# Kernel tuning notes

Measured on AMD Instinct MI355X. Metric: run time of the kernel, lower is better.

Reference implementation:

```python
import jax, jax.numpy as jnp
import numpy as np

N = 4096
IN_DIM = 256
HID = 64
HEADS = 4
OUT_DIM = 64
NEG = -9e15


def setup_inputs() -> dict:
    key = jax.random.key(0)
    ks = jax.random.split(key, 12)
    h = jax.random.normal(ks[0], (N, IN_DIM), dtype=jnp.float32)
    adj = jax.random.randint(ks[1], (N, N), 0, 2, dtype=jnp.int32)
    # per-head GATLayer params (W: Linear(input_dim, hid) with bias; a: Linear(2*hid, 1) with bias)
    Wh = jax.random.normal(ks[2], (HEADS, IN_DIM, HID), dtype=jnp.float32) * (1.414 / np.sqrt(IN_DIM + HID))
    bWh = jnp.zeros((HEADS, HID), dtype=jnp.float32)
    a_src = jax.random.normal(ks[3], (HEADS, HID), dtype=jnp.float32) * 0.1
    a_dst = jax.random.normal(ks[4], (HEADS, HID), dtype=jnp.float32) * 0.1
    a_b = jnp.zeros((HEADS,), dtype=jnp.float32)
    # output GATLayer params
    Wo = jax.random.normal(ks[5], (HEADS * HID, OUT_DIM), dtype=jnp.float32) * (1.414 / np.sqrt(HEADS * HID + OUT_DIM))
    bWo = jnp.zeros((OUT_DIM,), dtype=jnp.float32)
    ao_src = jax.random.normal(ks[6], (OUT_DIM,), dtype=jnp.float32) * 0.1
    ao_dst = jax.random.normal(ks[7], (OUT_DIM,), dtype=jnp.float32) * 0.1
    ao_b = jnp.zeros((), dtype=jnp.float32)
    return {"h": h, "adj": adj, "Wh": Wh, "bWh": bWh, "a_src": a_src, "a_dst": a_dst,
            "a_b": a_b, "Wo": Wo, "bWo": bWo, "ao_src": ao_src, "ao_dst": ao_dst, "ao_b": ao_b}


def _gat_layer(x, adj_mask, W, b, a_s, a_d, a_bias):
    # x: [N, F], W: [F, D]. Decompose a([wh_i || wh_j]) = a_s.wh_i + a_d.wh_j + a_bias
    wh = x @ W + b                                   # [N, D]
    s = (wh @ a_s)[:, None] + (wh @ a_d)[None, :] + a_bias  # [N, N]
    s = jax.nn.leaky_relu(s, negative_slope=0.2)
    s = jnp.where(adj_mask, s, NEG)
    att = jax.nn.softmax(s, axis=1)                  # softmax over neighbors j
    return att @ wh                                  # [N, D]


def reference(h, adj, Wh, bWh, a_src, a_dst, a_b, Wo, bWo, ao_src, ao_dst, ao_b):
    adj_mask = adj > 0
    # multi-head: vmap over stacked head params (dropout is identity in eval)
    heads = jax.vmap(lambda W, b, asr, ads, ab: _gat_layer(h, adj_mask, W, b, asr, ads, ab))(
        Wh, bWh, a_src, a_dst, a_b)                  # [H, N, D]
    out = jax.nn.elu(heads)
    out = jnp.transpose(out, (1, 0, 2)).reshape(N, HEADS * HID)  # concat heads
    out = _gat_layer(out, adj_mask, Wo, bWo, ao_src, ao_dst, ao_b)
    return jax.nn.elu(out)
```

## Files before the change

### kernel.cpp

```cpp
#include <hip/hip_runtime.h>

#define NN 4096
#define NHEADS 4
#define HID 64
#define INDIM 256

using short8 = __attribute__((ext_vector_type(8))) short;
using f32x4  = __attribute__((ext_vector_type(4))) float;

union f32u { float f; unsigned int u; };
union i4s8 { int4 i; short8 s; };

__device__ __forceinline__ float bf2f(unsigned short s) {
  f32u x; x.u = ((unsigned int)s) << 16; return x.f;
}
__device__ __forceinline__ unsigned short f2bf(float f) {
  f32u x; x.f = f;
  unsigned int r = x.u + 0x7fffu + ((x.u >> 16) & 1u);
  return (unsigned short)(r >> 16);
}
__device__ __forceinline__ unsigned int cvtpk(float lo, float hi) {
  unsigned int r;
  asm("v_cvt_pk_bf16_f32 %0, %1, %2" : "=v"(r) : "v"(lo), "v"(hi));
  return r;
}

__device__ __forceinline__ float ld(const unsigned short* p, size_t i) { return bf2f(p[i]); }
__device__ __forceinline__ float ld(const float* p, size_t i) { return p[i]; }
__device__ __forceinline__ void ld8(const unsigned short* p, float* out) {
  short8 v = *(const short8*)p;
#pragma unroll
  for (int j = 0; j < 8; j++) out[j] = bf2f((unsigned short)v[j]);
}
__device__ __forceinline__ void ld8(const float* p, float* out) {
  float4 a = *(const float4*)p;
  float4 b = *(const float4*)(p + 4);
  out[0] = a.x; out[1] = a.y; out[2] = a.z; out[3] = a.w;
  out[4] = b.x; out[5] = b.y; out[6] = b.z; out[7] = b.w;
}

__global__ __launch_bounds__(256) void k_probe(const void* hv, const void* adjv, int* flags) {
  __shared__ int s_bad, s_at;
  const int tid = threadIdx.x;
  if (tid == 0) { s_bad = 0; s_at = 0; }
  __syncthreads();
  const unsigned short* hu = (const unsigned short*)hv;
  float v = bf2f(hu[tid]);
  if (!(v > -1000.f && v < 1000.f)) atomicOr(&s_bad, 1);
  const unsigned int* au = (const unsigned int*)adjv;
  unsigned int wv = au[tid];
  if ((wv & 0xFFFFu) == 0x3F80u) atomicOr(&s_at, 2);
  else if (wv == 0x3F800000u) atomicOr(&s_at, 1);
  __syncthreads();
  if (tid == 0) {
    flags[0] = s_bad ? 0 : 1;
    int at = s_at;
    flags[1] = (at & 2) ? 2 : (at & 1);
  }
}

__global__ __launch_bounds__(256) void k_bm(const void* adjv, const int* __restrict__ flags,
                                            unsigned char* __restrict__ bm) {
  const int at = flags[1];
  const int i = blockIdx.x;
#pragma unroll
  for (int rep = 0; rep < 2; rep++) {
    int jb = threadIdx.x + rep * 256;
    unsigned int b = 0;
    if (at == 0) {
      const int4* arow = (const int4*)((const int*)adjv + (size_t)i * NN);
      int4 a0 = arow[jb * 2 + 0];
      int4 a1 = arow[jb * 2 + 1];
      b |= (a0.x > 0) ? 1u : 0u;  b |= (a0.y > 0) ? 2u : 0u;
      b |= (a0.z > 0) ? 4u : 0u;  b |= (a0.w > 0) ? 8u : 0u;
      b |= (a1.x > 0) ? 16u : 0u; b |= (a1.y > 0) ? 32u : 0u;
      b |= (a1.z > 0) ? 64u : 0u; b |= (a1.w > 0) ? 128u : 0u;
    } else if (at == 1) {
      const float* arow = (const float*)adjv + (size_t)i * NN + jb * 8;
      for (int t = 0; t < 8; t++) b |= (arow[t] > 0.5f) ? (1u << t) : 0u;
    } else {
      const unsigned short* arow = (const unsigned short*)adjv + (size_t)i * NN + jb * 8;
      for (int t = 0; t < 8; t++) b |= (bf2f(arow[t]) > 0.5f) ? (1u << t) : 0u;
    }
    bm[(size_t)i * 512 + jb] = (unsigned char)b;
  }
}

template <typename T>
__device__ __forceinline__ void wh_body(const T* h, const T* Wh, const T* bWh,
    const T* a_src, const T* a_dst, const T* a_b,
    unsigned short* Bp1, float* ssrc1, float* sdst1) {
  const int head = threadIdx.x >> 6;
  const int d = threadIdx.x & 63;
  const int i0 = blockIdx.x * 4;
  const T* W = Wh + (size_t)(head * INDIM) * HID + d;
  float acc[4];
  float bv = ld(bWh, head * HID + d);
#pragma unroll
  for (int r = 0; r < 4; r++) acc[r] = bv;
  for (int kb = 0; kb < INDIM / 8; kb++) {
    float wv[8];
#pragma unroll
    for (int j = 0; j < 8; j++) wv[j] = ld(W, (size_t)(kb * 8 + j) * HID);
#pragma unroll
    for (int r = 0; r < 4; r++) {
      float hf[8];
      ld8(h + (size_t)(i0 + r) * INDIM + kb * 8, hf);
#pragma unroll
      for (int j = 0; j < 8; j++) acc[r] = fmaf(hf[j], wv[j], acc[r]);
    }
  }
  float asv = ld(a_src, head * HID + d);
  float adv = ld(a_dst, head * HID + d);
  float abv = ld(a_b, head);
#pragma unroll
  for (int r = 0; r < 4; r++) {
    float ps = acc[r] * asv, pd = acc[r] * adv;
#pragma unroll
    for (int o = 32; o > 0; o >>= 1) { ps += __shfl_xor(ps, o); pd += __shfl_xor(pd, o); }
    int i = i0 + r;
    if (d == 0) { ssrc1[head * NN + i] = ps + abv; sdst1[head * NN + i] = pd; }
    int kb = i >> 5, quad = (i >> 3) & 3, jj = i & 7;
    int ln = quad * 16 + (d & 15), tt = d >> 4;
    Bp1[((((size_t)head * 128 + kb) * 4 + tt) * 64 + ln) * 8 + jj] = f2bf(acc[r]);
  }
}
__global__ __launch_bounds__(256) void k_wh(const void* h, const void* Wh, const void* bWh,
    const void* a_src, const void* a_dst, const void* a_b, const int* __restrict__ flags,
    unsigned short* Bp1, float* ssrc1, float* sdst1) {
  if (flags[0])
    wh_body<unsigned short>((const unsigned short*)h, (const unsigned short*)Wh,
        (const unsigned short*)bWh, (const unsigned short*)a_src,
        (const unsigned short*)a_dst, (const unsigned short*)a_b, Bp1, ssrc1, sdst1);
  else
    wh_body<float>((const float*)h, (const float*)Wh, (const float*)bWh, (const float*)a_src,
        (const float*)a_dst, (const float*)a_b, Bp1, ssrc1, sdst1);
}

__global__ __launch_bounds__(1024, 4) void k_att1s(
    const unsigned char* __restrict__ bm, const float* __restrict__ ssrc,
    const float* __restrict__ sdst, const short8* __restrict__ Bp,
    float* __restrict__ part, float* __restrict__ partl) {
  const int rb = blockIdx.x & 127;
  const int half = blockIdx.x >> 7;
  const int tid = threadIdx.x;
  const int w = tid >> 6;
  const int head = w & 3;
  const int sl = w >> 2;
  const int lane = tid & 63;
  const int r15 = lane & 15, quad = lane >> 4;
  const int row0 = rb * 32 + r15;
  const int row1 = row0 + 16;
  const float si0 = ssrc[head * NN + row0];
  const float si1 = ssrc[head * NN + row1];
  const unsigned char* bmr0 = bm + (size_t)row0 * 512;
  const unsigned char* bmr1 = bm + (size_t)row1 * 512;
  const float* sd = sdst + head * NN;
  const short8* Bh = Bp + (size_t)head * 128 * 4 * 64;
  f32x4 acc0[4], acc1[4];
#pragma unroll
  for (int t = 0; t < 4; t++) { acc0[t] = (f32x4){0,0,0,0}; acc1[t] = (f32x4){0,0,0,0}; }
  float ls0 = 0.f, ls1 = 0.f;
  const int kb0 = half * 64 + sl * 16;
  for (int g = 0; g < 4; g++) {
    const int kbg = kb0 + g * 4;
    int4 u0 = *(const int4*)(bmr0 + kbg * 4);
    int4 u1 = *(const int4*)(bmr1 + kbg * 4);
    int wd0[4] = {u0.x, u0.y, u0.z, u0.w};
    int wd1[4] = {u1.x, u1.y, u1.z, u1.w};
#pragma unroll
    for (int kk = 0; kk < 4; kk++) {
      const int kb = kbg + kk;
      const int j0 = kb * 32 + quad * 8;
      float4 q0 = *(const float4*)(sd + j0);
      float4 q1 = *(const float4*)(sd + j0 + 4);
      float sdv[8] = {q0.x, q0.y, q0.z, q0.w, q1.x, q1.y, q1.z, q1.w};
      unsigned int bits0 = (((unsigned int)wd0[kk]) >> (quad * 8)) & 0xffu;
      unsigned int bits1 = (((unsigned int)wd1[kk]) >> (quad * 8)) & 0xffu;
      float pe0[8], pe1[8];
#pragma unroll
      for (int jj = 0; jj < 8; jj++) {
        float t0 = si0 + sdv[jj];
        float e0 = __expf(fmaxf(t0, 0.2f * t0));
        pe0[jj] = ((bits0 >> jj) & 1u) ? e0 : 0.f;
        ls0 += pe0[jj];
        float t1 = si1 + sdv[jj];
        float e1 = __expf(fmaxf(t1, 0.2f * t1));
        pe1[jj] = ((bits1 >> jj) & 1u) ? e1 : 0.f;
        ls1 += pe1[jj];
      }
      i4s8 a0, a1;
      a0.i.x = cvtpk(pe0[0], pe0[1]); a0.i.y = cvtpk(pe0[2], pe0[3]);
      a0.i.z = cvtpk(pe0[4], pe0[5]); a0.i.w = cvtpk(pe0[6], pe0[7]);
      a1.i.x = cvtpk(pe1[0], pe1[1]); a1.i.y = cvtpk(pe1[2], pe1[3]);
      a1.i.z = cvtpk(pe1[4], pe1[5]); a1.i.w = cvtpk(pe1[6], pe1[7]);
      const short8* Bk = Bh + (size_t)kb * 256 + lane;
      short8 bt[4];
      bt[0] = Bk[0]; bt[1] = Bk[64]; bt[2] = Bk[128]; bt[3] = Bk[192];
#pragma unroll
      for (int t = 0; t < 4; t++) {
        acc0[t] = __builtin_amdgcn_mfma_f32_16x16x32_bf16(a0.s, bt[t], acc0[t], 0, 0, 0);
        acc1[t] = __builtin_amdgcn_mfma_f32_16x16x32_bf16(a1.s, bt[t], acc1[t], 0, 0, 0);
      }
    }
  }
  ls0 += __shfl_xor(ls0, 16); ls0 += __shfl_xor(ls0, 32);
  ls1 += __shfl_xor(ls1, 16); ls1 += __shfl_xor(ls1, 32);
  __shared__ float accs[8][16][66];
  __shared__ float lsh[8][16];
#define DOPASS(AC, LSV, PASS)                                                  \
  do {                                                                         \
    if (sl >= 2) {                                                             \
      const int slot = head * 2 + (sl - 2);                                    \
      if (lane < 16) lsh[slot][lane] = (LSV);                                  \
      _Pragma("unroll") for (int t = 0; t < 4; t++)                            \
        _Pragma("unroll") for (int gg = 0; gg < 4; gg++)                       \
          accs[slot][quad * 4 + gg][t * 16 + r15] = (AC)[t][gg];               \
    }                                                                          \
    __syncthreads();                                                           \
    if (sl < 2) {                                                              \
      const int slot = head * 2 + sl;                                          \
      if (lane < 16) lsh[slot][lane] += (LSV);                                 \
      _Pragma("unroll") for (int t = 0; t < 4; t++)                            \
        _Pragma("unroll") for (int gg = 0; gg < 4; gg++)                       \
          accs[slot][quad * 4 + gg][t * 16 + r15] += (AC)[t][gg];              \
    }                                                                          \
    __syncthreads();                                                           \
    _Pragma("unroll") for (int idx = tid; idx < 4096; idx += 1024) {           \
      int r = idx >> 8, hc = idx & 255;                                        \
      int hh = hc >> 6, col = hc & 63;                                         \
      part[((size_t)half * NN + rb * 32 + (PASS) * 16 + r) * 256 + hc] =       \
          accs[hh * 2][r][col] + accs[hh * 2 + 1][r][col];                     \
    }                                                                          \
    if (tid < 64)                                                              \
      partl[((size_t)half * 4 + (tid >> 4)) * NN + rb * 32 + (PASS) * 16 +     \
            (tid & 15)] = lsh[(tid >> 4) * 2][tid & 15] +                      \
                          lsh[(tid >> 4) * 2 + 1][tid & 15];                   \
    __syncthreads();                                                           \
  } while (0)
  DOPASS(acc0, ls0, 0);
  DOPASS(acc1, ls1, 1);
#undef DOPASS
}

__global__ __launch_bounds__(256) void k_att1f(const float* __restrict__ part,
    const float* __restrict__ partl, unsigned short* __restrict__ x2) {
  const int idx = blockIdx.x * 256 + threadIdx.x;
  const int row = idx >> 6;
  const int c4 = (idx & 63) * 4;
  const int head = c4 >> 6;
  const size_t off = (size_t)row * 256 + c4;
  float4 p0 = *(const float4*)(part + off);
  float4 p1 = *(const float4*)(part + (size_t)NN * 256 + off);
  float lt = partl[(size_t)head * NN + row] + partl[(size_t)(4 + head) * NN + row];
  float rl = (lt > 0.f) ? 1.f / lt : 0.f;
  float v0 = (p0.x + p1.x) * rl, v1 = (p0.y + p1.y) * rl;
  float v2 = (p0.z + p1.z) * rl, v3 = (p0.w + p1.w) * rl;
  v0 = v0 > 0.f ? v0 : __expf(v0) - 1.f;
  v1 = v1 > 0.f ? v1 : __expf(v1) - 1.f;
  v2 = v2 > 0.f ? v2 : __expf(v2) - 1.f;
  v3 = v3 > 0.f ? v3 : __expf(v3) - 1.f;
  uint2 st; st.x = cvtpk(v0, v1); st.y = cvtpk(v2, v3);
  *(uint2*)(x2 + off) = st;
}

__global__ __launch_bounds__(1024) void k_att1(
    const unsigned char* __restrict__ bm, const float* __restrict__ ssrc,
    const float* __restrict__ sdst, const short8* __restrict__ Bp,
    unsigned short* __restrict__ x2) {
  const int rb = blockIdx.x;
  const int tid = threadIdx.x;
  const int w = tid >> 6;
  const int head = w & 3;
  const int slice = w >> 2;
  const int lane = tid & 63;
  const int r15 = lane & 15, quad = lane >> 4;
  const int row = rb * 16 + r15;
  const float si = ssrc[head * NN + row];
  const unsigned char* bmrow = bm + (size_t)row * 512;
  const float* sd = sdst + head * NN;
  const short8* Bh = Bp + (size_t)head * 128 * 4 * 64;
  f32x4 acc0 = {0, 0, 0, 0}, acc1 = {0, 0, 0, 0}, acc2 = {0, 0, 0, 0}, acc3 = {0, 0, 0, 0};
  float lsum = 0.f;
  const int kb0 = slice * 32;
  for (int kb = kb0; kb < kb0 + 32; kb++) {
    const int j0 = kb * 32 + quad * 8;
    unsigned int bits = bmrow[kb * 4 + quad];
    float4 q0 = *(const float4*)(sd + j0);
    float4 q1 = *(const float4*)(sd + j0 + 4);
    float sdv[8] = {q0.x, q0.y, q0.z, q0.w, q1.x, q1.y, q1.z, q1.w};
    short8 af;
#pragma unroll
    for (int jj = 0; jj < 8; jj++) {
      float t = si + sdv[jj];
      float lr = fmaxf(t, 0.2f * t);
      float e = __expf(lr);
      float pe = ((bits >> jj) & 1u) ? e : 0.0f;
      lsum += pe;
      af[jj] = (short)f2bf(pe);
    }
    const short8* Bk = Bh + (size_t)kb * 256 + lane;
    short8 b0 = Bk[0], b1 = Bk[64], b2 = Bk[128], b3 = Bk[192];
    acc0 = __builtin_amdgcn_mfma_f32_16x16x32_bf16(af, b0, acc0, 0, 0, 0);
    acc1 = __builtin_amdgcn_mfma_f32_16x16x32_bf16(af, b1, acc1, 0, 0, 0);
    acc2 = __builtin_amdgcn_mfma_f32_16x16x32_bf16(af, b2, acc2, 0, 0, 0);
    acc3 = __builtin_amdgcn_mfma_f32_16x16x32_bf16(af, b3, acc3, 0, 0, 0);
  }
  lsum += __shfl_xor(lsum, 16);
  lsum += __shfl_xor(lsum, 32);
  __shared__ float accs[8][16][66];
  __shared__ float ls[8][16];
  if (slice >= 2) {
    const int slot = w - 8;
    if (lane < 16) ls[slot][lane] = lsum;
#pragma unroll
    for (int g = 0; g < 4; g++) {
      int r = quad * 4 + g;
      accs[slot][r][ 0 + r15] = acc0[g];
      accs[slot][r][16 + r15] = acc1[g];
      accs[slot][r][32 + r15] = acc2[g];
      accs[slot][r][48 + r15] = acc3[g];
    }
  }
  __syncthreads();
  if (slice < 2) {
    const int slot = w;
    if (lane < 16) ls[slot][lane] += lsum;
#pragma unroll
    for (int g = 0; g < 4; g++) {
      int r = quad * 4 + g;
      accs[slot][r][ 0 + r15] += acc0[g];
      accs[slot][r][16 + r15] += acc1[g];
      accs[slot][r][32 + r15] += acc2[g];
      accs[slot][r][48 + r15] += acc3[g];
    }
  }
  __syncthreads();
#pragma unroll
  for (int c = tid; c < 4096; c += 1024) {
    int r = c >> 8, hc = c & 255;
    int hh = hc >> 6, col = hc & 63;
    float s = accs[hh][r][col] + accs[hh + 4][r][col];
    float lt = ls[hh][r] + ls[hh + 4][r];
    float v = (lt > 0.f) ? s / lt : 0.f;
    v = v > 0.f ? v : __expf(v) - 1.f;
    x2[(size_t)(rb * 16 + r) * 256 + hc] = f2bf(v);
  }
}

template <typename T>
__device__ __forceinline__ void wo_body(const unsigned short* x2, const T* Wo, const T* bWo,
    const T* ao_src, const T* ao_dst, const T* ao_b,
    unsigned short* Bp2, float* ssrc2, float* sdst2) {
  const int w = threadIdx.x >> 6, d = threadIdx.x & 63;
  const int i = blockIdx.x * 4 + w;
  const short8* xr8 = (const short8*)(x2 + (size_t)i * 256);
  float acc = ld(bWo, d);
  for (int kb = 0; kb < 32; kb++) {
    float wv[8];
#pragma unroll
    for (int j = 0; j < 8; j++) wv[j] = ld(Wo, (size_t)(kb * 8 + j) * 64 + d);
    short8 xv = xr8[kb];
#pragma unroll
    for (int j = 0; j < 8; j++)
      acc = fmaf(bf2f((unsigned short)xv[j]), wv[j], acc);
  }
  float ps = acc * ld(ao_src, d);
  float pd = acc * ld(ao_dst, d);
#pragma unroll
  for (int o = 32; o > 0; o >>= 1) { ps += __shfl_xor(ps, o); pd += __shfl_xor(pd, o); }
  if (d == 0) { ssrc2[i] = ps + ld(ao_b, 0); sdst2[i] = pd; }
  int kb = i >> 5, quad = (i >> 3) & 3, jj = i & 7;
  int ln = quad * 16 + (d & 15), tt = d >> 4;
  Bp2[(((size_t)kb * 4 + tt) * 64 + ln) * 8 + jj] = f2bf(acc);
}
__global__ __launch_bounds__(256) void k_wo(const unsigned short* __restrict__ x2,
    const void* Wo, const void* bWo, const void* ao_src, const void* ao_dst, const void* ao_b,
    const int* __restrict__ flags, unsigned short* Bp2, float* ssrc2, float* sdst2) {
  if (flags[0])
    wo_body<unsigned short>(x2, (const unsigned short*)Wo, (const unsigned short*)bWo,
        (const unsigned short*)ao_src, (const unsigned short*)ao_dst,
        (const unsigned short*)ao_b, Bp2, ssrc2, sdst2);
  else
    wo_body<float>(x2, (const float*)Wo, (const float*)bWo, (const float*)ao_src,
        (const float*)ao_dst, (const float*)ao_b, Bp2, ssrc2, sdst2);
}

__global__ __launch_bounds__(1024) void k_att2(
    const unsigned char* __restrict__ bm, const float* __restrict__ ssrc,
    const float* __restrict__ sdst, const short8* __restrict__ Bp,
    const int* __restrict__ flags, void* __restrict__ outv) {
  const int rb = blockIdx.x;
  const int tid = threadIdx.x;
  const int w = tid >> 6;
  const int lane = tid & 63;
  const int r15 = lane & 15, quad = lane >> 4;
  const int row = rb * 16 + r15;
  const float si = ssrc[row];
  const unsigned char* bmrow = bm + (size_t)row * 512;
  f32x4 acc0 = {0, 0, 0, 0}, acc1 = {0, 0, 0, 0}, acc2 = {0, 0, 0, 0}, acc3 = {0, 0, 0, 0};
  float lsum = 0.f;
  const int kb0 = w * 8;
#pragma unroll
  for (int g = 0; g < 2; g++) {
    int4 ubm = *(const int4*)(bmrow + (kb0 + g * 4) * 4);
    int wds[4] = {ubm.x, ubm.y, ubm.z, ubm.w};
#pragma unroll
    for (int kk = 0; kk < 4; kk++) {
      const int kb = kb0 + g * 4 + kk;
      const int j0 = kb * 32 + quad * 8;
      unsigned int bits = (((unsigned int)wds[kk]) >> (quad * 8)) & 0xffu;
      float4 q0 = *(const float4*)(sdst + j0);
      float4 q1 = *(const float4*)(sdst + j0 + 4);
      float sdv[8] = {q0.x, q0.y, q0.z, q0.w, q1.x, q1.y, q1.z, q1.w};
      float pe[8];
#pragma unroll
      for (int jj = 0; jj < 8; jj++) {
        float t = si + sdv[jj];
        float e = __expf(fmaxf(t, 0.2f * t));
        pe[jj] = ((bits >> jj) & 1u) ? e : 0.f;
        lsum += pe[jj];
      }
      i4s8 a;
      a.i.x = cvtpk(pe[0], pe[1]); a.i.y = cvtpk(pe[2], pe[3]);
      a.i.z = cvtpk(pe[4], pe[5]); a.i.w = cvtpk(pe[6], pe[7]);
      const short8* Bk = Bp + (size_t)kb * 256 + lane;
      short8 b0 = Bk[0], b1 = Bk[64], b2 = Bk[128], b3 = Bk[192];
      acc0 = __builtin_amdgcn_mfma_f32_16x16x32_bf16(a.s, b0, acc0, 0, 0, 0);
      acc1 = __builtin_amdgcn_mfma_f32_16x16x32_bf16(a.s, b1, acc1, 0, 0, 0);
      acc2 = __builtin_amdgcn_mfma_f32_16x16x32_bf16(a.s, b2, acc2, 0, 0, 0);
      acc3 = __builtin_amdgcn_mfma_f32_16x16x32_bf16(a.s, b3, acc3, 0, 0, 0);
    }
  }
  lsum += __shfl_xor(lsum, 16);
  lsum += __shfl_xor(lsum, 32);
  __shared__ float accs[8][16][66];
  __shared__ float ls2[8][16];
  if (w >= 8) {
    const int slot = w - 8;
    if (lane < 16) ls2[slot][lane] = lsum;
#pragma unroll
    for (int g = 0; g < 4; g++) {
      int r = quad * 4 + g;
      accs[slot][r][ 0 + r15] = acc0[g];
      accs[slot][r][16 + r15] = acc1[g];
      accs[slot][r][32 + r15] = acc2[g];
      accs[slot][r][48 + r15] = acc3[g];
    }
  }
  __syncthreads();
  if (w < 8) {
    const int slot = w;
    if (lane < 16) ls2[slot][lane] += lsum;
#pragma unroll
    for (int g = 0; g < 4; g++) {
      int r = quad * 4 + g;
      accs[slot][r][ 0 + r15] += acc0[g];
      accs[slot][r][16 + r15] += acc1[g];
      accs[slot][r][32 + r15] += acc2[g];
      accs[slot][r][48 + r15] += acc3[g];
    }
  }
  __syncthreads();
  {
    const int r = tid >> 6, col = tid & 63;
    float s = 0.f, lt = 0.f;
#pragma unroll
    for (int k = 0; k < 8; k++) { s += accs[k][r][col]; lt += ls2[k][r]; }
    float v = (lt > 0.f) ? s / lt : 0.f;
    v = v > 0.f ? v : __expf(v) - 1.f;
    size_t idx = (size_t)(rb * 16 + r) * 64 + col;
    if (flags[0]) ((unsigned short*)outv)[idx] = f2bf(v);
    else          ((float*)outv)[idx] = v;
  }
}

extern "C" void kernel_launch(void* const* d_in, const int* in_sizes, int n_in,
                              void* d_out, int out_size, void* d_ws, size_t ws_size,
                              hipStream_t stream) {
  const void* h      = d_in[0];
  const void* adj    = d_in[1];
  const void* Wh     = d_in[2];
  const void* bWh    = d_in[3];
  const void* a_src  = d_in[4];
  const void* a_dst  = d_in[5];
  const void* a_b    = d_in[6];
  const void* Wo     = d_in[7];
  const void* bWo    = d_in[8];
  const void* ao_src = d_in[9];
  const void* ao_dst = d_in[10];
  const void* ao_b   = d_in[11];

  size_t need_old = 16 + (size_t)NN * 512 + (size_t)NHEADS * NN * HID * 2 +
                    (size_t)NN * 256 * 2 + (size_t)NN * 64 * 2 +
                    (size_t)NHEADS * NN * 8 + (size_t)NN * 8;
  size_t need_new = need_old + (size_t)2 * NN * 256 * 4 + (size_t)2 * 4 * NN * 4;
  hipMemsetAsync(d_out, 0x41, (size_t)out_size * 2, stream);
  if (ws_size < need_old) {
    hipMemsetAsync(d_out, 0x45, (size_t)out_size * 2, stream);
    return;
  }
  const bool big = ws_size >= need_new;
  unsigned char* ws = (unsigned char*)d_ws;
  int* flags = (int*)ws;                        ws += 16;
  unsigned char* bmp = ws;                      ws += (size_t)NN * 512;
  unsigned short* Bp1 = (unsigned short*)ws;    ws += (size_t)NHEADS * NN * HID * 2;
  unsigned short* x2  = (unsigned short*)ws;    ws += (size_t)NN * 256 * 2;
  unsigned short* Bp2 = (unsigned short*)ws;    ws += (size_t)NN * 64 * 2;
  float* ssrc1 = (float*)ws;                    ws += (size_t)NHEADS * NN * 4;
  float* sdst1 = (float*)ws;                    ws += (size_t)NHEADS * NN * 4;
  float* ssrc2 = (float*)ws;                    ws += (size_t)NN * 4;
  float* sdst2 = (float*)ws;                    ws += (size_t)NN * 4;
  float* part  = (float*)ws;                    ws += (size_t)2 * NN * 256 * 4;
  float* partl = (float*)ws;                    ws += (size_t)2 * 4 * NN * 4;

  k_probe<<<dim3(1),    dim3(256),  0, stream>>>(h, adj, flags);
  k_bm   <<<dim3(4096), dim3(256),  0, stream>>>(adj, flags, bmp);
  k_wh   <<<dim3(1024), dim3(256),  0, stream>>>(h, Wh, bWh, a_src, a_dst, a_b, flags,
                                                 Bp1, ssrc1, sdst1);
  if (big) {
    k_att1s<<<dim3(256),  dim3(1024), 0, stream>>>(bmp, ssrc1, sdst1, (const short8*)Bp1,
                                                   part, partl);
    k_att1f<<<dim3(1024), dim3(256),  0, stream>>>(part, partl, x2);
  } else {
    k_att1<<<dim3(256), dim3(1024), 0, stream>>>(bmp, ssrc1, sdst1, (const short8*)Bp1, x2);
  }
  k_wo   <<<dim3(1024), dim3(256),  0, stream>>>(x2, Wo, bWo, ao_src, ao_dst, ao_b, flags,
                                                 Bp2, ssrc2, sdst2);
  k_att2 <<<dim3(256),  dim3(1024), 0, stream>>>(bmp, ssrc2, sdst2, (const short8*)Bp2,
                                                 flags, d_out);
}
```

Baseline: 219.1 us.

## Restructure projection kernels with split-K across waves and 16-row tiles

Both linear projection kernels (k_wh and k_wo) now give each 1024-thread block 16 rows and split the K dimension across four wave groups. Partial sums are reduced through shared memory. Bf16 packed B-operand tiles are written as 16-byte vector stores, and the attention-score dot products are computed from shared memory instead of wave shuffles. The aim is more reuse of each weight load across rows and fewer narrow scattered stores, at the cost of extra LDS traffic, two block barriers, and fewer blocks (256).

```diff
diff --git a/kernel.cpp b/kernel.cpp
--- a/kernel.cpp
+++ b/kernel.cpp
@@ -89,52 +89,85 @@
 template <typename T>
 __device__ __forceinline__ void wh_body(const T* h, const T* Wh, const T* bWh,
     const T* a_src, const T* a_dst, const T* a_b,
-    unsigned short* Bp1, float* ssrc1, float* sdst1) {
-  const int head = threadIdx.x >> 6;
-  const int d = threadIdx.x & 63;
-  const int i0 = blockIdx.x * 4;
-  const T* W = Wh + (size_t)(head * INDIM) * HID + d;
-  float acc[4];
-  float bv = ld(bWh, head * HID + d);
-#pragma unroll
-  for (int r = 0; r < 4; r++) acc[r] = bv;
-  for (int kb = 0; kb < INDIM / 8; kb++) {
+    unsigned short* __restrict__ Bp1, float* __restrict__ ssrc1, float* __restrict__ sdst1,
+    float (*wp)[16][260], float* av0, float* av1) {
+  const int tid = threadIdx.x;
+  const int w = tid >> 6, lane = tid & 63;
+  const int head = w & 3, kq = w >> 2;
+  const int rb = blockIdx.x;
+  const int R0 = rb * 16;
+  const int d = lane;
+  if (tid < 256) av0[tid] = ld(a_src, tid);
+  else if (tid < 512) av1[tid - 256] = ld(a_dst, tid - 256);
+  float acc[16];
+  float bv = (kq == 0) ? ld(bWh, head * 64 + d) : 0.f;
+#pragma unroll
+  for (int r = 0; r < 16; r++) acc[r] = bv;
+  const int k0 = kq * 64;
+  for (int kb = 0; kb < 8; kb++) {
     float wv[8];
 #pragma unroll
-    for (int j = 0; j < 8; j++) wv[j] = ld(W, (size_t)(kb * 8 + j) * HID);
-#pragma unroll
-    for (int r = 0; r < 4; r++) {
+    for (int j = 0; j < 8; j++)
+      wv[j] = ld(Wh, (size_t)(head * 256 + k0 + kb * 8 + j) * 64 + d);
+#pragma unroll
+    for (int r = 0; r < 16; r++) {
       float hf[8];
-      ld8(h + (size_t)(i0 + r) * INDIM + kb * 8, hf);
+      ld8(h + (size_t)(R0 + r) * 256 + k0 + kb * 8, hf);
 #pragma unroll
       for (int j = 0; j < 8; j++) acc[r] = fmaf(hf[j], wv[j], acc[r]);
     }
   }
-  float asv = ld(a_src, head * HID + d);
-  float adv = ld(a_dst, head * HID + d);
-  float abv = ld(a_b, head);
-#pragma unroll
-  for (int r = 0; r < 4; r++) {
-    float ps = acc[r] * asv, pd = acc[r] * adv;
-#pragma unroll
-    for (int o = 32; o > 0; o >>= 1) { ps += __shfl_xor(ps, o); pd += __shfl_xor(pd, o); }
-    int i = i0 + r;
-    if (d == 0) { ssrc1[head * NN + i] = ps + abv; sdst1[head * NN + i] = pd; }
-    int kb = i >> 5, quad = (i >> 3) & 3, jj = i & 7;
-    int ln = quad * 16 + (d & 15), tt = d >> 4;
-    Bp1[((((size_t)head * 128 + kb) * 4 + tt) * 64 + ln) * 8 + jj] = f2bf(acc[r]);
-  }
-}
-__global__ __launch_bounds__(256) void k_wh(const void* h, const void* Wh, const void* bWh,
+  if (kq >= 2) {
+#pragma unroll
+    for (int r = 0; r < 16; r++) wp[kq - 2][r][head * 64 + d] = acc[r];
+  }
+  __syncthreads();
+  if (kq < 2) {
+#pragma unroll
+    for (int r = 0; r < 16; r++) wp[kq][r][head * 64 + d] += acc[r];
+  }
+  __syncthreads();
+  if (tid < 512) {
+    const int hh = tid >> 7, tt = (tid >> 5) & 3, lnh = tid & 31;
+    const int q2 = (rb & 1) * 2 + (lnh >> 4);
+    const int ln = q2 * 16 + (lnh & 15);
+    const int dd = tt * 16 + (lnh & 15);
+    const int rbase = (lnh >> 4) * 8;
+    float v[8];
+#pragma unroll
+    for (int jj = 0; jj < 8; jj++)
+      v[jj] = wp[0][rbase + jj][hh * 64 + dd] + wp[1][rbase + jj][hh * 64 + dd];
+    i4s8 s;
+    s.i.x = cvtpk(v[0], v[1]); s.i.y = cvtpk(v[2], v[3]);
+    s.i.z = cvtpk(v[4], v[5]); s.i.w = cvtpk(v[6], v[7]);
+    const int kb = rb >> 1;
+    *(int4*)(Bp1 + ((((size_t)hh * 128 + kb) * 4 + tt) * 64 + ln) * 8) = s.i;
+  } else if (tid < 576) {
+    const int t2 = tid - 512;
+    const int hh = t2 >> 4, r = t2 & 15;
+    float ps = 0.f, pd = 0.f;
+    for (int c = 0; c < 64; c++) {
+      float wv2 = wp[0][r][hh * 64 + c] + wp[1][r][hh * 64 + c];
+      ps = fmaf(wv2, av0[hh * 64 + c], ps);
+      pd = fmaf(wv2, av1[hh * 64 + c], pd);
+    }
+    ssrc1[hh * NN + R0 + r] = ps + ld(a_b, hh);
+    sdst1[hh * NN + R0 + r] = pd;
+  }
+}
+__global__ __launch_bounds__(1024, 4) void k_wh(const void* h, const void* Wh, const void* bWh,
     const void* a_src, const void* a_dst, const void* a_b, const int* __restrict__ flags,
     unsigned short* Bp1, float* ssrc1, float* sdst1) {
+  __shared__ float wp[2][16][260];
+  __shared__ float av0[256], av1[256];
   if (flags[0])
     wh_body<unsigned short>((const unsigned short*)h, (const unsigned short*)Wh,
         (const unsigned short*)bWh, (const unsigned short*)a_src,
-        (const unsigned short*)a_dst, (const unsigned short*)a_b, Bp1, ssrc1, sdst1);
+        (const unsigned short*)a_dst, (const unsigned short*)a_b, Bp1, ssrc1, sdst1,
+        wp, av0, av1);
   else
     wh_body<float>((const float*)h, (const float*)Wh, (const float*)bWh, (const float*)a_src,
-        (const float*)a_dst, (const float*)a_b, Bp1, ssrc1, sdst1);
+        (const float*)a_dst, (const float*)a_b, Bp1, ssrc1, sdst1, wp, av0, av1);
 }
 
 __global__ __launch_bounds__(1024, 4) void k_att1s(
@@ -351,39 +384,84 @@
 template <typename T>
 __device__ __forceinline__ void wo_body(const unsigned short* x2, const T* Wo, const T* bWo,
     const T* ao_src, const T* ao_dst, const T* ao_b,
-    unsigned short* Bp2, float* ssrc2, float* sdst2) {
-  const int w = threadIdx.x >> 6, d = threadIdx.x & 63;
-  const int i = blockIdx.x * 4 + w;
-  const short8* xr8 = (const short8*)(x2 + (size_t)i * 256);
-  float acc = ld(bWo, d);
-  for (int kb = 0; kb < 32; kb++) {
+    unsigned short* __restrict__ Bp2, float* __restrict__ ssrc2, float* __restrict__ sdst2,
+    float (*wp)[16][68], float* av) {
+  const int tid = threadIdx.x;
+  const int w = tid >> 6, lane = tid & 63;
+  const int rg = w & 3, kq = w >> 2;
+  const int rb = blockIdx.x;
+  const int R0 = rb * 16 + rg * 4;
+  const int d = lane;
+  if (tid < 64) av[tid] = ld(ao_src, tid);
+  else if (tid < 128) av[tid] = ld(ao_dst, tid - 64);
+  float acc[4];
+  float bv = (kq == 0) ? ld(bWo, d) : 0.f;
+#pragma unroll
+  for (int r = 0; r < 4; r++) acc[r] = bv;
+  const int k0 = kq * 64;
+  for (int kb = 0; kb < 8; kb++) {
     float wv[8];
 #pragma unroll
-    for (int j = 0; j < 8; j++) wv[j] = ld(Wo, (size_t)(kb * 8 + j) * 64 + d);
-    short8 xv = xr8[kb];
-#pragma unroll
     for (int j = 0; j < 8; j++)
-      acc = fmaf(bf2f((unsigned short)xv[j]), wv[j], acc);
-  }
-  float ps = acc * ld(ao_src, d);
-  float pd = acc * ld(ao_dst, d);
-#pragma unroll
-  for (int o = 32; o > 0; o >>= 1) { ps += __shfl_xor(ps, o); pd += __shfl_xor(pd, o); }
-  if (d == 0) { ssrc2[i] = ps + ld(ao_b, 0); sdst2[i] = pd; }
-  int kb = i >> 5, quad = (i >> 3) & 3, jj = i & 7;
-  int ln = quad * 16 + (d & 15), tt = d >> 4;
-  Bp2[(((size_t)kb * 4 + tt) * 64 + ln) * 8 + jj] = f2bf(acc);
-}
-__global__ __launch_bounds__(256) void k_wo(const unsigned short* __restrict__ x2,
+      wv[j] = ld(Wo, (size_t)(k0 + kb * 8 + j) * 64 + d);
+#pragma unroll
+    for (int r = 0; r < 4; r++) {
+      float hf[8];
+      ld8(x2 + (size_t)(R0 + r) * 256 + k0 + kb * 8, hf);
+#pragma unroll
+      for (int j = 0; j < 8; j++) acc[r] = fmaf(hf[j], wv[j], acc[r]);
+    }
+  }
+  const int rr = rg * 4;
+  if (kq >= 2) {
+#pragma unroll
+    for (int r = 0; r < 4; r++) wp[kq - 2][rr + r][d] = acc[r];
+  }
+  __syncthreads();
+  if (kq < 2) {
+#pragma unroll
+    for (int r = 0; r < 4; r++) wp[kq][rr + r][d] += acc[r];
+  }
+  __syncthreads();
+  if (tid < 128) {
+    const int tt = tid >> 5, lnh = tid & 31;
+    const int q2 = (rb & 1) * 2 + (lnh >> 4);
+    const int ln = q2 * 16 + (lnh & 15);
+    const int dd = tt * 16 + (lnh & 15);
+    const int rbase = (lnh >> 4) * 8;
+    float v[8];
+#pragma unroll
+    for (int jj = 0; jj < 8; jj++)
+      v[jj] = wp[0][rbase + jj][dd] + wp[1][rbase + jj][dd];
+    i4s8 s;
+    s.i.x = cvtpk(v[0], v[1]); s.i.y = cvtpk(v[2], v[3]);
+    s.i.z = cvtpk(v[4], v[5]); s.i.w = cvtpk(v[6], v[7]);
+    const int kb = rb >> 1;
+    *(int4*)(Bp2 + (((size_t)kb * 4 + tt) * 64 + ln) * 8) = s.i;
+  } else if (tid < 144) {
+    const int r = tid - 128;
+    float ps = 0.f, pd = 0.f;
+    for (int c = 0; c < 64; c++) {
+      float wv2 = wp[0][r][c] + wp[1][r][c];
+      ps = fmaf(wv2, av[c], ps);
+      pd = fmaf(wv2, av[64 + c], pd);
+    }
+    ssrc2[(size_t)rb * 16 + r] = ps + ld(ao_b, 0);
+    sdst2[(size_t)rb * 16 + r] = pd;
+  }
+}
+__global__ __launch_bounds__(1024, 4) void k_wo(const unsigned short* __restrict__ x2,
     const void* Wo, const void* bWo, const void* ao_src, const void* ao_dst, const void* ao_b,
     const int* __restrict__ flags, unsigned short* Bp2, float* ssrc2, float* sdst2) {
+  __shared__ float wp[2][16][68];
+  __shared__ float av[128];
   if (flags[0])
     wo_body<unsigned short>(x2, (const unsigned short*)Wo, (const unsigned short*)bWo,
         (const unsigned short*)ao_src, (const unsigned short*)ao_dst,
-        (const unsigned short*)ao_b, Bp2, ssrc2, sdst2);
+        (const unsigned short*)ao_b, Bp2, ssrc2, sdst2, wp, av);
   else
     wo_body<float>(x2, (const float*)Wo, (const float*)bWo, (const float*)ao_src,
-        (const float*)ao_dst, (const float*)ao_b, Bp2, ssrc2, sdst2);
+        (const float*)ao_dst, (const float*)ao_b, Bp2, ssrc2, sdst2, wp, av);
 }
 
 __global__ __launch_bounds__(1024) void k_att2(
@@ -516,7 +594,7 @@
 
   k_probe<<<dim3(1),    dim3(256),  0, stream>>>(h, adj, flags);
   k_bm   <<<dim3(4096), dim3(256),  0, stream>>>(adj, flags, bmp);
-  k_wh   <<<dim3(1024), dim3(256),  0, stream>>>(h, Wh, bWh, a_src, a_dst, a_b, flags,
+  k_wh   <<<dim3(256),  dim3(1024), 0, stream>>>(h, Wh, bWh, a_src, a_dst, a_b, flags,
                                                  Bp1, ssrc1, sdst1);
   if (big) {
     k_att1s<<<dim3(256),  dim3(1024), 0, stream>>>(bmp, ssrc1, sdst1, (const short8*)Bp1,
@@ -525,7 +603,7 @@
   } else {
     k_att1<<<dim3(256), dim3(1024), 0, stream>>>(bmp, ssrc1, sdst1, (const short8*)Bp1, x2);
   }
-  k_wo   <<<dim3(1024), dim3(256),  0, stream>>>(x2, Wo, bWo, ao_src, ao_dst, ao_b, flags,
+  k_wo   <<<dim3(256),  dim3(1024), 0, stream>>>(x2, Wo, bWo, ao_src, ao_dst, ao_b, flags,
                                                  Bp2, ssrc2, sdst2);
   k_att2 <<<dim3(256),  dim3(1024), 0, stream>>>(bmp, ssrc2, sdst2, (const short8*)Bp2,
                                                  flags, d_out);
```

Result: faster. 207.9 us (-5.1%).
